# Optimization experiments

Measured on AMD Instinct MI355X. Metric: run time of the kernel, lower is better.

## Reference

```python
import jax, jax.numpy as jnp
import numpy as np

TOP_K = 2


def setup_inputs() -> dict:
    key = jax.random.key(0)
    k1, k2 = jax.random.split(key)
    hidden_states = jax.random.normal(k1, (4, 8192, 4096), dtype=jnp.float32)
    # xavier_uniform for Linear(4096 -> 64): bound = sqrt(6/(fan_in+fan_out))
    bound = float(np.sqrt(6.0 / (4096 + 64)))
    gate_w = jax.random.uniform(k2, (64, 4096), dtype=jnp.float32, minval=-bound, maxval=bound)
    return {"hidden_states": hidden_states, "gate_w": gate_w}


def reference(hidden_states, gate_w):
    # Flatten [B, S, H] -> [T, H]
    H = hidden_states.shape[-1]
    x = hidden_states.reshape(-1, H)
    # Gate projection: [T, H] @ [H, E] -> [T, E]
    router_logits = jnp.einsum('th,eh->te', x, gate_w)
    # Top-k expert selection (eval mode: no noise)
    top_k_logits, top_k_indices = jax.lax.top_k(router_logits, TOP_K)
    # Normalize selected weights with a softmax over the k logits
    top_k_weights = jax.nn.softmax(top_k_logits, axis=-1)
    return top_k_weights, top_k_indices, router_logits
```

## Files before the change

### kernel.cpp

```cpp
#include <hip/hip_runtime.h>


#define NT    256
#define TT    32768
#define HD    4096
#define NE    64
#define BKT   32
#define NKT   128
#define BUFB  25600
#define ALIM  ((size_t)TT * HD * 4 - 16)

typedef __attribute__((ext_vector_type(8))) short bf16x8;
typedef __attribute__((ext_vector_type(4))) float f32x4;

#define MFMA __builtin_amdgcn_mfma_f32_16x16x32_bf16

__device__ __forceinline__ bf16x8 u2b(uint4 u) { return __builtin_bit_cast(bf16x8, u); }
__device__ __forceinline__ float4 b4f(uint4 u) { return __builtin_bit_cast(float4, u); }

__device__ __forceinline__ void gload_lds16(const void* g, void* l) {
  __builtin_amdgcn_global_load_lds(
      (const __attribute__((address_space(1))) void*)g,
      (__attribute__((address_space(3))) void*)l, 16, 0, 0);
}

__device__ __forceinline__ void tsplit8(float4 a, float4 b,
                                        uint4& o0, uint4& o1, uint4& o2) {
  float f[8] = {a.x, a.y, a.z, a.w, b.x, b.y, b.z, b.w};
  unsigned p0[4], p1[4], p2[4];
#pragma unroll
  for (int j = 0; j < 4; ++j) {
    float x0 = f[2 * j], x1 = f[2 * j + 1];
    unsigned u0 = __float_as_uint(x0) & 0xffff0000u;
    unsigned u1 = __float_as_uint(x1) & 0xffff0000u;
    float r0 = x0 - __uint_as_float(u0);
    float r1 = x1 - __uint_as_float(u1);
    unsigned v0 = __float_as_uint(r0) & 0xffff0000u;
    unsigned v1 = __float_as_uint(r1) & 0xffff0000u;
    float s0 = r0 - __uint_as_float(v0);
    float s1 = r1 - __uint_as_float(v1);
    p0[j] = (u0 >> 16) | u1;
    p1[j] = (v0 >> 16) | v1;
    p2[j] = (__float_as_uint(s0) >> 16) | (__float_as_uint(s1) & 0xffff0000u);
  }
  o0 = make_uint4(p0[0], p0[1], p0[2], p0[3]);
  o1 = make_uint4(p1[0], p1[1], p1[2], p1[3]);
  o2 = make_uint4(p2[0], p2[1], p2[2], p2[3]);
}

__global__ __launch_bounds__(256)
void prepack_w_kernel(const float* __restrict__ W, uint4* __restrict__ Bp) {
  const int t  = blockIdx.x * 256 + threadIdx.x;
  const int e  = t >> 9;
  const int k0 = (t & 511) * 8;
  const float4* wp = (const float4*)(W + (size_t)e * HD + k0);
  uint4 o0, o1, o2;
  tsplit8(wp[0], wp[1], o0, o1, o2);
  const int ts = k0 >> 5;
  const int lg = (k0 >> 3) & 3;
  const int f  = e >> 4;
  const int ln = lg * 16 + (e & 15);
  Bp[(((ts * 3 + 0) * 4 + f) << 6) + ln] = o0;
  Bp[(((ts * 3 + 1) * 4 + f) << 6) + ln] = o1;
  Bp[(((ts * 3 + 2) * 4 + f) << 6) + ln] = o2;
}

#define PROD1(AM0, AM1, BN0, BN1) \
    acc00 = MFMA(AM0, BN0, acc00, 0, 0, 0); \
    acc01 = MFMA(AM0, BN1, acc01, 0, 0, 0); \
    acc10 = MFMA(AM1, BN0, acc10, 0, 0, 0); \
    acc11 = MFMA(AM1, BN1, acc11, 0, 0, 0);

__global__ __launch_bounds__(NT, 2)
void router_dma_kernel(const float* __restrict__ A, const uint4* __restrict__ Bp,
                       float* __restrict__ outw, float* __restrict__ outi,
                       float* __restrict__ outl) {
  __shared__ __align__(16) unsigned char smem[2 * BUFB];

  const int tid  = threadIdx.x;
  const int bm   = blockIdx.x;
  const int lane = tid & 63;
  const int w    = tid >> 6;
  const int wr   = w >> 1;
  const int wc   = w & 1;
  const int l15  = lane & 15;
  const int lg   = lane >> 4;

  const char* Abytes = (const char*)A;

  size_t srcoff[7];
#pragma unroll
  for (int j = 0; j < 7; ++j) {
    int ii = j * 4 + w;
    int f  = ii * 1024 + lane * 16;
    int r  = f / 400, rb = f % 400;
    srcoff[j] = (size_t)(bm * 64 + r) * (HD * 4) + (size_t)(rb < 384 ? rb : 0);
  }

#define DMA_ISSUE(CT, BOFF) { \
    _Pragma("unroll") \
    for (int j = 0; j < 7; ++j) { \
      int ii = j * 4 + w; \
      if (ii < 25) { \
        size_t off = srcoff[j] + (size_t)(CT) * 384; \
        if (off > ALIM) off -= (size_t)(HD * 4); \
        gload_lds16(Abytes + off, smem + (BOFF) + ii * 1024); \
      } \
    } \
    __builtin_amdgcn_sched_barrier(0); }

  const int row0b = (wr * 32 + l15) * 400;
  const int row1b = row0b + 16 * 400;
  const int lgb   = lg * 32;

  const uint4* pbB = Bp + wc * 128 + lane;

  f32x4 acc00 = {0.f,0.f,0.f,0.f}, acc01 = {0.f,0.f,0.f,0.f};
  f32x4 acc10 = {0.f,0.f,0.f,0.f}, acc11 = {0.f,0.f,0.f,0.f};

  uint4 bA0f0, bA0f1, bA1f0, bA1f1, bA2f0, bA2f1;
  uint4 bB0f0, bB0f1, bB1f0, bB1f1, bB2f0, bB2f1;

#define LOADB(SET, G) { \
    const uint4* q_ = pbB + (size_t)(G) * 768; \
    SET##0f0 = q_[0];   SET##0f1 = q_[64]; \
    SET##1f0 = q_[256]; SET##1f1 = q_[320]; \
    SET##2f0 = q_[512]; SET##2f1 = q_[576]; }

#define BSTEP(BOFF, S, BU, BL, GN, DOLOAD) { \
    if (DOLOAD) { LOADB(BL, GN) } \
    uint4 rA0lo = *(const uint4*)(smem + (BOFF) + row0b + (S) * 128 + lgb); \
    uint4 rA0hi = *(const uint4*)(smem + (BOFF) + row0b + (S) * 128 + lgb + 16); \
    uint4 rA1lo = *(const uint4*)(smem + (BOFF) + row1b + (S) * 128 + lgb); \
    uint4 rA1hi = *(const uint4*)(smem + (BOFF) + row1b + (S) * 128 + lgb + 16); \
    uint4 x0, x1, x2, y0, y1, y2; \
    tsplit8(b4f(rA0lo), b4f(rA0hi), x0, x1, x2); \
    tsplit8(b4f(rA1lo), b4f(rA1hi), y0, y1, y2); \
    const bf16x8 a0m0 = u2b(x0), a1m0 = u2b(x1), a2m0 = u2b(x2); \
    const bf16x8 a0m1 = u2b(y0), a1m1 = u2b(y1), a2m1 = u2b(y2); \
    PROD1(a0m0, a0m1, u2b(BU##2f0), u2b(BU##2f1)) \
    PROD1(a1m0, a1m1, u2b(BU##1f0), u2b(BU##1f1)) \
    PROD1(a2m0, a2m1, u2b(BU##0f0), u2b(BU##0f1)) \
    PROD1(a0m0, a0m1, u2b(BU##1f0), u2b(BU##1f1)) \
    PROD1(a1m0, a1m1, u2b(BU##0f0), u2b(BU##0f1)) \
    PROD1(a0m0, a0m1, u2b(BU##0f0), u2b(BU##0f1)) }

  DMA_ISSUE(0, 0)
  LOADB(bA, 0)
  __syncthreads();

#pragma unroll 1
  for (int ot = 0; ot < 21; ++ot) {
    const int g0 = ot * 6;
    DMA_ISSUE(2 * ot + 1, BUFB)
    BSTEP(0, 0, bA, bB, g0 + 1, true)
    BSTEP(0, 1, bB, bA, g0 + 2, true)
    BSTEP(0, 2, bA, bB, g0 + 3, true)
    __syncthreads();
    DMA_ISSUE(2 * ot + 2, 0)
    BSTEP(BUFB, 0, bB, bA, g0 + 4, true)
    BSTEP(BUFB, 1, bA, bB, g0 + 5, true)
    BSTEP(BUFB, 2, bB, bA, g0 + 6, true)
    __syncthreads();
  }

  BSTEP(0, 0, bA, bB, 127, true)
  BSTEP(0, 1, bB, bA, 0, false)

  const int t0 = bm * 64;
  float* lf = (float*)smem;

  __syncthreads();

#define EPO(MI, NI, ACC) \
  { _Pragma("unroll") \
    for (int r = 0; r < 4; ++r) { \
      int tl = wr * 32 + (MI) * 16 + lg * 4 + r; \
      int e  = wc * 32 + (NI) * 16 + l15; \
      float v = ACC[r]; \
      outl[(size_t)(t0 + tl) * NE + e] = v; \
      lf[tl * 65 + e] = v; \
    } }
  EPO(0, 0, acc00) EPO(0, 1, acc01) EPO(1, 0, acc10) EPO(1, 1, acc11)
#undef EPO

  __syncthreads();

  if (tid < 64) {
    const int t = tid;
    float m1 = -1e30f, m2 = -1e30f;
    int i1 = 0, i2 = 0;
#pragma unroll
    for (int e = 0; e < NE; ++e) {
      float v = lf[t * 65 + e];
      if (v > m1)      { m2 = m1; i2 = i1; m1 = v; i1 = e; }
      else if (v > m2) { m2 = v; i2 = e; }
    }
    float e2  = expf(m2 - m1);
    float inv = 1.0f / (1.0f + e2);
    outw[(size_t)(t0 + t) * 2 + 0] = inv;
    outw[(size_t)(t0 + t) * 2 + 1] = e2 * inv;
    outi[(size_t)(t0 + t) * 2 + 0] = (float)i1;
    outi[(size_t)(t0 + t) * 2 + 1] = (float)i2;
  }
}

__global__ __launch_bounds__(256, 2)
void topk_router_lds(const float* __restrict__ A, const float* __restrict__ W,
                     float* __restrict__ outw, float* __restrict__ outi,
                     float* __restrict__ outl) {
  __shared__ __align__(16) unsigned char smem[49152];
  const int tid  = threadIdx.x;
  const int bm   = blockIdx.x;
  const int lane = tid & 63;
  const int wid  = tid >> 6;
  const int wr   = wid >> 1;
  const int wc   = wid & 1;
  const int l15  = lane & 15;
  const int lg   = lane >> 4;
  const int s_r  = tid >> 2;
  const int s_cb = (tid & 3) << 3;
  const float* aball = A + (size_t)(bm * 64 + s_r) * HD + s_cb;
  const float* bball = W + (size_t)s_r * HD + s_cb;
  const unsigned wswz  = ((unsigned)((s_r >> 1) & 3)) << 4;
  const unsigned wbyte = (unsigned)(s_r * 64) + (((unsigned)(s_cb * 2)) ^ wswz);
  f32x4 acc00 = {0.f,0.f,0.f,0.f}, acc01 = {0.f,0.f,0.f,0.f};
  f32x4 acc10 = {0.f,0.f,0.f,0.f}, acc11 = {0.f,0.f,0.f,0.f};
  float4 aE0, aE1, bE0, bE1, aO0, aO1, bO0, bO1;
#define LOADS(T, A0, A1, B0, B1) { \
    const float4* ap = (const float4*)(aball + (size_t)(T) * BKT); \
    A0 = ap[0]; A1 = ap[1]; \
    const float4* bp = (const float4*)(bball + (size_t)(T) * BKT); \
    B0 = bp[0]; B1 = bp[1]; }
#define CONVW2(BB, A0, A1, B0, B1) { \
    uint4 o0, o1, o2; \
    tsplit8(A0, A1, o0, o1, o2); \
    *(uint4*)(smem + (BB) +     0 + wbyte) = o0; \
    *(uint4*)(smem + (BB) +  4096 + wbyte) = o1; \
    *(uint4*)(smem + (BB) +  8192 + wbyte) = o2; \
    tsplit8(B0, B1, o0, o1, o2); \
    *(uint4*)(smem + (BB) + 12288 + wbyte) = o0; \
    *(uint4*)(smem + (BB) + 16384 + wbyte) = o1; \
    *(uint4*)(smem + (BB) + 20480 + wbyte) = o2; }
  auto compute = [&](int bb) {
    bf16x8 a0m0, a0m1, a1m0, a1m1, a2m0, a2m1;
    bf16x8 b0n0, b0n1, b1n0, b1n1, b2n0, b2n1;
    const unsigned kb = (unsigned)(lg * 16);
#define LDA(SI, MI, DST) { \
    int row = wr * 32 + (MI) * 16 + l15; \
    DST = *(const bf16x8*)(smem + bb + (SI) * 4096 + row * 64 + \
          (kb ^ ((((unsigned)row >> 1) & 3) << 4))); }
#define LDB(SI, NI, DST) { \
    int row = wc * 32 + (NI) * 16 + l15; \
    DST = *(const bf16x8*)(smem + bb + 12288 + (SI) * 4096 + row * 64 + \
          (kb ^ ((((unsigned)row >> 1) & 3) << 4))); }
    LDA(0, 0, a0m0) LDA(0, 1, a0m1)
    LDA(1, 0, a1m0) LDA(1, 1, a1m1)
    LDA(2, 0, a2m0) LDA(2, 1, a2m1)
    LDB(0, 0, b0n0) LDB(0, 1, b0n1)
    LDB(1, 0, b1n0) LDB(1, 1, b1n1)
    LDB(2, 0, b2n0) LDB(2, 1, b2n1)
#undef LDA
#undef LDB
    PROD1(a0m0, a0m1, b2n0, b2n1)
    PROD1(a1m0, a1m1, b1n0, b1n1)
    PROD1(a2m0, a2m1, b0n0, b0n1)
    PROD1(a0m0, a0m1, b1n0, b1n1)
    PROD1(a1m0, a1m1, b0n0, b0n1)
    PROD1(a0m0, a0m1, b0n0, b0n1)
  };
  LOADS(0, aE0, aE1, bE0, bE1)
  LOADS(1, aO0, aO1, bO0, bO1)
  CONVW2(0, aE0, aE1, bE0, bE1)
  __syncthreads();
#pragma unroll 1
  for (int kk = 0; kk < NKT; kk += 2) {
    if (kk + 2 < NKT) { LOADS(kk + 2, aE0, aE1, bE0, bE1) }
    __builtin_amdgcn_sched_barrier(0);
    compute(0);
    CONVW2(24576, aO0, aO1, bO0, bO1)
    __syncthreads();
    if (kk + 3 < NKT) { LOADS(kk + 3, aO0, aO1, bO0, bO1) }
    __builtin_amdgcn_sched_barrier(0);
    compute(24576);
    if (kk + 2 < NKT) { CONVW2(0, aE0, aE1, bE0, bE1) }
    __syncthreads();
  }
  const int t0 = bm * 64;
  float* lf2 = (float*)smem;
#define EPI(MI, NI, ACC) \
  { _Pragma("unroll") \
    for (int r = 0; r < 4; ++r) { \
      int tl = wr * 32 + (MI) * 16 + lg * 4 + r; \
      int e  = wc * 32 + (NI) * 16 + l15; \
      float v = ACC[r]; \
      outl[(size_t)(t0 + tl) * NE + e] = v; \
      lf2[tl * 65 + e] = v; \
    } }
  EPI(0, 0, acc00) EPI(0, 1, acc01) EPI(1, 0, acc10) EPI(1, 1, acc11)
#undef EPI
  __syncthreads();
  if (tid < 64) {
    const int t = tid;
    float m1 = -1e30f, m2 = -1e30f;
    int i1 = 0, i2 = 0;
#pragma unroll
    for (int e = 0; e < NE; ++e) {
      float v = lf2[t * 65 + e];
      if (v > m1)      { m2 = m1; i2 = i1; m1 = v; i1 = e; }
      else if (v > m2) { m2 = v; i2 = e; }
    }
    float e2  = expf(m2 - m1);
    float inv = 1.0f / (1.0f + e2);
    outw[(size_t)(t0 + t) * 2 + 0] = inv;
    outw[(size_t)(t0 + t) * 2 + 1] = e2 * inv;
    outi[(size_t)(t0 + t) * 2 + 0] = (float)i1;
    outi[(size_t)(t0 + t) * 2 + 1] = (float)i2;
  }
}

extern "C" void kernel_launch(void* const* d_in, const int* in_sizes, int n_in,
                              void* d_out, int out_size, void* d_ws, size_t ws_size,
                              hipStream_t stream) {
  (void)in_sizes; (void)n_in; (void)out_size;
  const float* A = (const float*)d_in[0];
  const float* W = (const float*)d_in[1];
  float* outw = (float*)d_out;
  float* outi = (float*)d_out + 2 * TT;
  float* outl = (float*)d_out + 4 * TT;

  const size_t need = (size_t)NKT * 3 * 4 * 1024;
  if (ws_size >= need) {
    hipLaunchKernelGGL(prepack_w_kernel, dim3(128), dim3(256), 0, stream,
                       W, (uint4*)d_ws);
    hipLaunchKernelGGL(router_dma_kernel, dim3(TT / 64), dim3(NT), 0, stream,
                       A, (const uint4*)d_ws, outw, outi, outl);
  } else {
    hipLaunchKernelGGL(topk_router_lds, dim3(TT / 64), dim3(256), 0, stream,
                       A, W, outw, outi, outl);
  }
}
```

Before: 172.5 us.

## Triple-buffer A tiles with XOR-swizzled DMA and vmcnt-based pipelining

Replaces the double-buffered, padded-row (400B) direct-to-LDS load of A with a three-buffer ring of 64-row by 64-float tiles. Tiles are stored with an XOR swizzle so LDS reads avoid bank conflicts without padding. Synchronisation now uses an explicit vmcnt wait plus s_barrier per stage instead of full __syncthreads, keeping two DMA stages in flight. Prepacked W fragments for two k-substeps are register double-buffered. This aims to hide HBM latency in a bandwidth-bound kernel and to drop the out-of-range address clamping, at the cost of more registers and LDS and a fragile hand-tuned waitcnt.

```diff
diff --git a/kernel.cpp b/kernel.cpp
--- a/kernel.cpp
+++ b/kernel.cpp
@@ -5,10 +5,9 @@
 #define TT    32768
 #define HD    4096
 #define NE    64
-#define BKT   32
-#define NKT   128
-#define BUFB  25600
-#define ALIM  ((size_t)TT * HD * 4 - 16)
+#define NST   64
+#define BUFB  16384u
+#define NBUF  3
 
 typedef __attribute__((ext_vector_type(8))) short bf16x8;
 typedef __attribute__((ext_vector_type(4))) float f32x4;
@@ -72,10 +71,10 @@
     acc11 = MFMA(AM1, BN1, acc11, 0, 0, 0);
 
 __global__ __launch_bounds__(NT, 2)
-void router_dma_kernel(const float* __restrict__ A, const uint4* __restrict__ Bp,
-                       float* __restrict__ outw, float* __restrict__ outi,
-                       float* __restrict__ outl) {
-  __shared__ __align__(16) unsigned char smem[2 * BUFB];
+void router_pipe_kernel(const float* __restrict__ A, const uint4* __restrict__ Bp,
+                        float* __restrict__ outw, float* __restrict__ outi,
+                        float* __restrict__ outl) {
+  __shared__ __align__(16) unsigned char smem[NBUF * BUFB];
 
   const int tid  = threadIdx.x;
   const int bm   = blockIdx.x;
@@ -85,92 +84,102 @@
   const int wc   = w & 1;
   const int l15  = lane & 15;
   const int lg   = lane >> 4;
-
-  const char* Abytes = (const char*)A;
-
-  size_t srcoff[7];
+  const int x7   = l15 & 7;
+
+  const char* Ab = (const char*)A;
+
+  unsigned soff[4];
 #pragma unroll
-  for (int j = 0; j < 7; ++j) {
-    int ii = j * 4 + w;
-    int f  = ii * 1024 + lane * 16;
-    int r  = f / 400, rb = f % 400;
-    srcoff[j] = (size_t)(bm * 64 + r) * (HD * 4) + (size_t)(rb < 384 ? rb : 0);
-  }
-
-#define DMA_ISSUE(CT, BOFF) { \
+  for (int j = 0; j < 4; ++j) {
+    int rj = w * 16 + j * 4 + lg;
+    int gs = l15 ^ (rj & 7);
+    soff[j] = (unsigned)((bm * 64 + rj) * (HD * 4)) + (unsigned)(gs * 16);
+  }
+
+#define DMA(T, BD) { \
+    const int tc_ = (T) > (NST - 1) ? (NST - 1) : (T); \
     _Pragma("unroll") \
-    for (int j = 0; j < 7; ++j) { \
-      int ii = j * 4 + w; \
-      if (ii < 25) { \
-        size_t off = srcoff[j] + (size_t)(CT) * 384; \
-        if (off > ALIM) off -= (size_t)(HD * 4); \
-        gload_lds16(Abytes + off, smem + (BOFF) + ii * 1024); \
-      } \
-    } \
-    __builtin_amdgcn_sched_barrier(0); }
-
-  const int row0b = (wr * 32 + l15) * 400;
-  const int row1b = row0b + 16 * 400;
-  const int lgb   = lg * 32;
+    for (int j = 0; j < 4; ++j) \
+      gload_lds16(Ab + (size_t)soff[j] + (size_t)tc_ * 256, \
+                  smem + (BD) + (unsigned)((w * 4 + j) * 1024)); }
 
   const uint4* pbB = Bp + wc * 128 + lane;
+
+#define LOADB(P, T) { \
+    const int tc_ = (T) > (NST - 1) ? (NST - 1) : (T); \
+    const uint4* q_ = pbB + (size_t)tc_ * 1536; \
+    P##s0L0f0 = q_[0];    P##s0L0f1 = q_[64]; \
+    P##s0L1f0 = q_[256];  P##s0L1f1 = q_[320]; \
+    P##s0L2f0 = q_[512];  P##s0L2f1 = q_[576]; \
+    P##s1L0f0 = q_[768];  P##s1L0f1 = q_[832]; \
+    P##s1L1f0 = q_[1024]; P##s1L1f1 = q_[1088]; \
+    P##s1L2f0 = q_[1280]; P##s1L2f1 = q_[1344]; }
+
+  uint4 Es0L0f0, Es0L0f1, Es0L1f0, Es0L1f1, Es0L2f0, Es0L2f1;
+  uint4 Es1L0f0, Es1L0f1, Es1L1f0, Es1L1f1, Es1L2f0, Es1L2f1;
+  uint4 Os0L0f0, Os0L0f1, Os0L1f0, Os0L1f1, Os0L2f0, Os0L2f1;
+  uint4 Os1L0f0, Os1L0f1, Os1L1f0, Os1L1f1, Os1L2f0, Os1L2f1;
 
   f32x4 acc00 = {0.f,0.f,0.f,0.f}, acc01 = {0.f,0.f,0.f,0.f};
   f32x4 acc10 = {0.f,0.f,0.f,0.f}, acc11 = {0.f,0.f,0.f,0.f};
 
-  uint4 bA0f0, bA0f1, bA1f0, bA1f1, bA2f0, bA2f1;
-  uint4 bB0f0, bB0f1, bB1f0, bB1f1, bB2f0, bB2f1;
-
-#define LOADB(SET, G) { \
-    const uint4* q_ = pbB + (size_t)(G) * 768; \
-    SET##0f0 = q_[0];   SET##0f1 = q_[64]; \
-    SET##1f0 = q_[256]; SET##1f1 = q_[320]; \
-    SET##2f0 = q_[512]; SET##2f1 = q_[576]; }
-
-#define BSTEP(BOFF, S, BU, BL, GN, DOLOAD) { \
-    if (DOLOAD) { LOADB(BL, GN) } \
-    uint4 rA0lo = *(const uint4*)(smem + (BOFF) + row0b + (S) * 128 + lgb); \
-    uint4 rA0hi = *(const uint4*)(smem + (BOFF) + row0b + (S) * 128 + lgb + 16); \
-    uint4 rA1lo = *(const uint4*)(smem + (BOFF) + row1b + (S) * 128 + lgb); \
-    uint4 rA1hi = *(const uint4*)(smem + (BOFF) + row1b + (S) * 128 + lgb + 16); \
-    uint4 x0, x1, x2, y0, y1, y2; \
-    tsplit8(b4f(rA0lo), b4f(rA0hi), x0, x1, x2); \
-    tsplit8(b4f(rA1lo), b4f(rA1hi), y0, y1, y2); \
-    const bf16x8 a0m0 = u2b(x0), a1m0 = u2b(x1), a2m0 = u2b(x2); \
-    const bf16x8 a0m1 = u2b(y0), a1m1 = u2b(y1), a2m1 = u2b(y2); \
-    PROD1(a0m0, a0m1, u2b(BU##2f0), u2b(BU##2f1)) \
-    PROD1(a1m0, a1m1, u2b(BU##1f0), u2b(BU##1f1)) \
-    PROD1(a2m0, a2m1, u2b(BU##0f0), u2b(BU##0f1)) \
-    PROD1(a0m0, a0m1, u2b(BU##1f0), u2b(BU##1f1)) \
-    PROD1(a1m0, a1m1, u2b(BU##0f0), u2b(BU##0f1)) \
-    PROD1(a0m0, a0m1, u2b(BU##0f0), u2b(BU##0f1)) }
-
-  DMA_ISSUE(0, 0)
-  LOADB(bA, 0)
+  const unsigned r0base = (unsigned)((wr * 32 + l15) * 256);
+
+#define BSTEPX(BC, S, B0f0, B0f1, B1f0, B1f1, B2f0, B2f1) { \
+    const int gi_ = (S) * 8 + lg * 2; \
+    const unsigned glo_ = (unsigned)((gi_ ^ x7) << 4); \
+    const unsigned ghi_ = (unsigned)(((gi_ + 1) ^ x7) << 4); \
+    const unsigned char* b0_ = smem + (BC) + r0base; \
+    const unsigned char* b1_ = b0_ + 16 * 256; \
+    uint4 a0lo = *(const uint4*)(b0_ + glo_); \
+    uint4 a0hi = *(const uint4*)(b0_ + ghi_); \
+    uint4 a1lo = *(const uint4*)(b1_ + glo_); \
+    uint4 a1hi = *(const uint4*)(b1_ + ghi_); \
+    uint4 x0_, x1_, x2_, y0_, y1_, y2_; \
+    tsplit8(b4f(a0lo), b4f(a0hi), x0_, x1_, x2_); \
+    tsplit8(b4f(a1lo), b4f(a1hi), y0_, y1_, y2_); \
+    const bf16x8 a0m0 = u2b(x0_), a1m0 = u2b(x1_), a2m0 = u2b(x2_); \
+    const bf16x8 a0m1 = u2b(y0_), a1m1 = u2b(y1_), a2m1 = u2b(y2_); \
+    PROD1(a0m0, a0m1, u2b(B2f0), u2b(B2f1)) \
+    PROD1(a1m0, a1m1, u2b(B1f0), u2b(B1f1)) \
+    PROD1(a2m0, a2m1, u2b(B0f0), u2b(B0f1)) \
+    PROD1(a0m0, a0m1, u2b(B1f0), u2b(B1f1)) \
+    PROD1(a1m0, a1m1, u2b(B0f0), u2b(B0f1)) \
+    PROD1(a0m0, a0m1, u2b(B0f0), u2b(B0f1)) }
+
+#define COMPUTE2(BC, P) \
+    BSTEPX(BC, 0, P##s0L0f0, P##s0L0f1, P##s0L1f0, P##s0L1f1, P##s0L2f0, P##s0L2f1) \
+    BSTEPX(BC, 1, P##s1L0f0, P##s1L0f1, P##s1L1f0, P##s1L1f1, P##s1L2f0, P##s1L2f1)
+
+#define HALF(ST, LOADSET, COMPSET) { \
+    asm volatile("s_waitcnt vmcnt(16)" ::: "memory"); \
+    __builtin_amdgcn_s_barrier(); \
+    __builtin_amdgcn_sched_barrier(0); \
+    LOADB(LOADSET, (ST) + 1) \
+    DMA((ST) + 2, bd) \
+    __builtin_amdgcn_sched_barrier(0); \
+    COMPUTE2(bc, COMPSET) \
+    bc += BUFB; if (bc == NBUF * BUFB) bc = 0; \
+    bd += BUFB; if (bd == NBUF * BUFB) bd = 0; }
+
+  DMA(0, 0u)
+  asm volatile("" ::: "memory");
+  LOADB(E, 0)
+  DMA(1, BUFB)
+
+  unsigned bc = 0, bd = 2 * BUFB;
+
+#pragma unroll 1
+  for (int p = 0; p < NST / 2; ++p) {
+    HALF(2 * p,     O, E)
+    HALF(2 * p + 1, E, O)
+  }
+
+  asm volatile("s_waitcnt vmcnt(0)" ::: "memory");
   __syncthreads();
-
-#pragma unroll 1
-  for (int ot = 0; ot < 21; ++ot) {
-    const int g0 = ot * 6;
-    DMA_ISSUE(2 * ot + 1, BUFB)
-    BSTEP(0, 0, bA, bB, g0 + 1, true)
-    BSTEP(0, 1, bB, bA, g0 + 2, true)
-    BSTEP(0, 2, bA, bB, g0 + 3, true)
-    __syncthreads();
-    DMA_ISSUE(2 * ot + 2, 0)
-    BSTEP(BUFB, 0, bB, bA, g0 + 4, true)
-    BSTEP(BUFB, 1, bA, bB, g0 + 5, true)
-    BSTEP(BUFB, 2, bB, bA, g0 + 6, true)
-    __syncthreads();
-  }
-
-  BSTEP(0, 0, bA, bB, 127, true)
-  BSTEP(0, 1, bB, bA, 0, false)
 
   const int t0 = bm * 64;
   float* lf = (float*)smem;
-
-  __syncthreads();
 
 #define EPO(MI, NI, ACC) \
   { _Pragma("unroll") \
@@ -228,9 +237,9 @@
   f32x4 acc10 = {0.f,0.f,0.f,0.f}, acc11 = {0.f,0.f,0.f,0.f};
   float4 aE0, aE1, bE0, bE1, aO0, aO1, bO0, bO1;
 #define LOADS(T, A0, A1, B0, B1) { \
-    const float4* ap = (const float4*)(aball + (size_t)(T) * BKT); \
+    const float4* ap = (const float4*)(aball + (size_t)(T) * 32); \
     A0 = ap[0]; A1 = ap[1]; \
-    const float4* bp = (const float4*)(bball + (size_t)(T) * BKT); \
+    const float4* bp = (const float4*)(bball + (size_t)(T) * 32); \
     B0 = bp[0]; B1 = bp[1]; }
 #define CONVW2(BB, A0, A1, B0, B1) { \
     uint4 o0, o1, o2; \
@@ -274,16 +283,16 @@
   CONVW2(0, aE0, aE1, bE0, bE1)
   __syncthreads();
 #pragma unroll 1
-  for (int kk = 0; kk < NKT; kk += 2) {
-    if (kk + 2 < NKT) { LOADS(kk + 2, aE0, aE1, bE0, bE1) }
+  for (int kk = 0; kk < 128; kk += 2) {
+    if (kk + 2 < 128) { LOADS(kk + 2, aE0, aE1, bE0, bE1) }
     __builtin_amdgcn_sched_barrier(0);
     compute(0);
     CONVW2(24576, aO0, aO1, bO0, bO1)
     __syncthreads();
-    if (kk + 3 < NKT) { LOADS(kk + 3, aO0, aO1, bO0, bO1) }
+    if (kk + 3 < 128) { LOADS(kk + 3, aO0, aO1, bO0, bO1) }
     __builtin_amdgcn_sched_barrier(0);
     compute(24576);
-    if (kk + 2 < NKT) { CONVW2(0, aE0, aE1, bE0, bE1) }
+    if (kk + 2 < 128) { CONVW2(0, aE0, aE1, bE0, bE1) }
     __syncthreads();
   }
   const int t0 = bm * 64;
@@ -329,11 +338,11 @@
   float* outi = (float*)d_out + 2 * TT;
   float* outl = (float*)d_out + 4 * TT;
 
-  const size_t need = (size_t)NKT * 3 * 4 * 1024;
+  const size_t need = (size_t)128 * 3 * 4 * 1024;
   if (ws_size >= need) {
     hipLaunchKernelGGL(prepack_w_kernel, dim3(128), dim3(256), 0, stream,
                        W, (uint4*)d_ws);
-    hipLaunchKernelGGL(router_dma_kernel, dim3(TT / 64), dim3(NT), 0, stream,
+    hipLaunchKernelGGL(router_pipe_kernel, dim3(TT / 64), dim3(NT), 0, stream,
                        A, (const uint4*)d_ws, outw, outi, outl);
   } else {
     hipLaunchKernelGGL(topk_router_lds, dim3(TT / 64), dim3(256), 0, stream,
```

Measured after the change: 170.3 us. About the same (-1.2%).
